# Kernel optimization log

Measured on AMD Instinct MI355X. Metric: run time of the kernel, lower is better.

## Reference

```python
import jax, jax.numpy as jnp
import numpy as np

SLOPE = 25.0   # fast_sigmoid surrogate slope
BETA = 0.9     # LIF decay
THR = 1.0      # snntorch default threshold
STEPS = 10


@jax.custom_vjp
def spike(x):
    # Heaviside forward, fast-sigmoid surrogate backward
    return (x > 0).astype(x.dtype)

def _spike_fwd(x):
    return spike(x), x

def _spike_bwd(x, g):
    return (g / (SLOPE * jnp.abs(x) + 1.0) ** 2,)

spike.defvjp(_spike_fwd, _spike_bwd)


def lif(inp, mem):
    # snntorch Leaky, reset_mechanism='subtract': reset based on previous mem, detached
    reset = jax.lax.stop_gradient((mem > THR).astype(mem.dtype))
    mem = BETA * mem + inp - reset * THR
    spk = spike(mem - THR)
    return spk, mem


def setup_inputs() -> dict:
    key = jax.random.key(0)
    ks = jax.random.split(key, 4)
    B, IN, H, O = 65536, 512, 1024, 1
    x = jax.random.normal(ks[0], (B, IN), dtype=jnp.float32)
    W1 = jax.random.normal(ks[1], (IN, H), dtype=jnp.float32) / np.sqrt(IN)
    b1 = jnp.zeros((H,), jnp.float32)
    W2 = jax.random.normal(ks[2], (H, H), dtype=jnp.float32) / np.sqrt(H)
    b2 = jnp.zeros((H,), jnp.float32)
    Wo = jax.random.normal(ks[3], (H, O), dtype=jnp.float32) / np.sqrt(H)
    bo = jnp.zeros((O,), jnp.float32)
    return {"x": x, "W1": W1, "b1": b1, "W2": W2, "b2": b2, "Wo": Wo, "bo": bo}


def reference(x, W1, b1, W2, b2, Wo, bo):
    # fc1(x) is identical every timestep (x is static input current)
    cur1 = x @ W1 + b1                      # [B, H]
    B = x.shape[0]
    H = W1.shape[1]
    O = Wo.shape[1]
    m1 = jnp.zeros((B, H), x.dtype)
    m2 = jnp.zeros((B, H), x.dtype)
    mo = jnp.zeros((B, O), x.dtype)

    def step(carry, _):
        m1, m2, mo = carry
        s1, m1 = lif(cur1, m1)
        s2, m2 = lif(s1 @ W2 + b2, m2)
        _, mo = lif(s2 @ Wo + bo, mo)
        return (m1, m2, mo), mo

    _, recs = jax.lax.scan(step, (m1, m2, mo), None, length=STEPS)  # [STEPS, B, O]
    return recs.mean(0)
```

## Files before the change

kernel.cpp:

```cpp
#include <hip/hip_runtime.h>
#include <cstdint>
#include <cstddef>


typedef _Float16 f16;
typedef _Float16 f16x8 __attribute__((ext_vector_type(8)));
typedef float f32x4 __attribute__((ext_vector_type(4)));
typedef int i32x4 __attribute__((ext_vector_type(4)));

#define MFMA16(A, B, C) __builtin_amdgcn_mfma_f32_16x16x32_f16(A, B, C, 0, 0, 0)

static constexpr int BSZ = 65536;
static constexpr int IN = 512;
static constexpr int H = 1024;

__global__ void prep_dekker(const float* __restrict__ src, f16* __restrict__ dst) {
    int idx = blockIdx.x * 256 + threadIdx.x;
    int k = idx >> 10;
    int j = idx & 1023;
    float w = src[(size_t)k * 1024 + j];
    f16 hi = (f16)w;
    float lo = (w - (float)hi) * 2048.0f;
    size_t o = (size_t)j * 1024 + k;
    dst[o] = hi;
    dst[o + (size_t)H * H] = (f16)lo;
}

__global__ __launch_bounds__(256, 2) void k1_chain(
    const float* __restrict__ x, const float* __restrict__ w1,
    const float* __restrict__ b1, unsigned short* __restrict__ s1b) {
    __shared__ float xs[32][132];
    __shared__ float ws[32][256];
    const int hblk = blockIdx.x;
    const int bblk = blockIdx.y;
    const int tid = threadIdx.x;
    const int ht = tid & 15, bt = tid >> 4;
    const int h0 = hblk * 256, b0 = bblk * 128;

    float acc[8][16] = {};

    float4 xv[4], wv[8];
#pragma unroll
    for (int i = 0; i < 4; ++i) {
        int idx = tid + 256 * i;
        int br = idx >> 3, ks = idx & 7;
        xv[i] = *(const float4*)&x[(size_t)(b0 + br) * IN + ks * 4];
    }
#pragma unroll
    for (int i = 0; i < 8; ++i) {
        int idx = tid + 256 * i;
        int kr = idx >> 6, c4 = idx & 63;
        wv[i] = *(const float4*)&w1[(size_t)kr * H + h0 + c4 * 4];
    }

    for (int kc = 0; kc < 512; kc += 32) {
        __syncthreads();
#pragma unroll
        for (int i = 0; i < 4; ++i) {
            int idx = tid + 256 * i;
            int br = idx >> 3, ks = idx & 7;
            xs[ks * 4 + 0][br] = xv[i].x;
            xs[ks * 4 + 1][br] = xv[i].y;
            xs[ks * 4 + 2][br] = xv[i].z;
            xs[ks * 4 + 3][br] = xv[i].w;
        }
#pragma unroll
        for (int i = 0; i < 8; ++i) {
            int idx = tid + 256 * i;
            int kr = idx >> 6, c4 = idx & 63;
            *(float4*)&ws[kr][c4 * 4] = wv[i];
        }
        __syncthreads();
        int kn = (kc + 32) & 511;
#pragma unroll
        for (int i = 0; i < 4; ++i) {
            int idx = tid + 256 * i;
            int br = idx >> 3, ks = idx & 7;
            xv[i] = *(const float4*)&x[(size_t)(b0 + br) * IN + kn + ks * 4];
        }
#pragma unroll
        for (int i = 0; i < 8; ++i) {
            int idx = tid + 256 * i;
            int kr = idx >> 6, c4 = idx & 63;
            wv[i] = *(const float4*)&w1[(size_t)(kn + kr) * H + h0 + c4 * 4];
        }
#pragma unroll 2
        for (int k = 0; k < 32; ++k) {
            float xr[8];
            *(float4*)&xr[0] = *(const float4*)&xs[k][bt * 8];
            *(float4*)&xr[4] = *(const float4*)&xs[k][bt * 8 + 4];
            float wr[16];
#pragma unroll
            for (int g = 0; g < 4; ++g)
                *(float4*)&wr[g * 4] = *(const float4*)&ws[k][ht * 4 + 64 * g];
#pragma unroll
            for (int i = 0; i < 8; ++i)
#pragma unroll
                for (int j = 0; j < 16; ++j)
                    acc[i][j] = fmaf(xr[i], wr[j], acc[i][j]);
        }
    }

    float b1v[16];
#pragma unroll
    for (int g = 0; g < 4; ++g)
#pragma unroll
        for (int m = 0; m < 4; ++m)
            b1v[g * 4 + m] = b1[h0 + g * 64 + ht * 4 + m];
#pragma unroll
    for (int i = 0; i < 8; ++i) {
        unsigned short outb[16];
#pragma unroll
        for (int j = 0; j < 16; ++j) {
            float c = __fadd_rn(acc[i][j], b1v[j]);
            float m = 0.0f;
            unsigned bits = 0u;
#pragma unroll
            for (int t = 0; t < 10; ++t) {
                float rst = (m > 1.0f) ? 1.0f : 0.0f;
                m = __fmul_rn(0.9f, m);
                m = __fadd_rn(m, c);
                m = __fsub_rn(m, rst);
                if (m > 1.0f) bits |= (1u << t);
            }
            outb[j] = (unsigned short)bits;
        }
        size_t row = (size_t)(b0 + bt * 8 + i);
#pragma unroll
        for (int g = 0; g < 4; ++g)
            *(int2*)&s1b[row * H + h0 + g * 64 + ht * 4] = ((const int2*)outb)[g];
    }
}

__global__ __launch_bounds__(512, 4) void k2_spikes_gemm(
    const unsigned short* __restrict__ s1bits, const f16* __restrict__ w2d,
    const float* __restrict__ b2, const float* __restrict__ wo,
    float* __restrict__ po) {
    __shared__ i32x4 AL[2][2][4][64];
    __shared__ i32x4 BL[2][2][2][2][64];
    __shared__ float m2x[4][64][8];
    const int jblk = blockIdx.x, bblk = blockIdx.y;
    const int tid = threadIdx.x;
    const int lane = tid & 63, wave = tid >> 6;
    const int strip = wave & 3, thalf = wave >> 2;
    const int l15 = lane & 15, loct = lane >> 4;
    const int t0 = thalf * 5;

    const bool stageB = (tid >= 256);
    const int s = tid & 255;
    const int sl15 = s & 15, sseg = (s >> 4) & 3;
    const int slot = (sseg << 4) | sl15;
    const int astrip = s >> 6;
    const int bp = (s >> 7) & 1, bcf = (s >> 6) & 1;

    const char* gsrc;
    if (stageB)
        gsrc = (const char*)(w2d + (size_t)bp * H * H
                             + (size_t)(jblk * 32 + bcf * 16 + sl15) * 1024 + sseg * 8);
    else
        gsrc = (const char*)(s1bits + (size_t)(bblk * 64 + astrip * 16 + sl15) * 1024 + sseg * 8);

    f32x4 acc[5][2][2] = {};

    i32x4 gv0 = *(const i32x4*)(gsrc);
    i32x4 gv1 = *(const i32x4*)(gsrc + 64);

    typedef union { i32x4 i; unsigned long long u[2]; f16x8 h; } U;

    int buf = 0;
    for (int kc = 0; kc < 1024; kc += 64) {
        if (stageB) {
            BL[buf][0][bp][bcf][slot] = gv0;
            BL[buf][1][bp][bcf][slot] = gv1;
        } else {
            AL[buf][0][astrip][slot] = gv0;
            AL[buf][1][astrip][slot] = gv1;
        }
        int kn = (kc + 64) & 1023;
        i32x4 gn0 = *(const i32x4*)(gsrc + kn * 2);
        i32x4 gn1 = *(const i32x4*)(gsrc + kn * 2 + 64);
        asm volatile("s_waitcnt lgkmcnt(0)" ::: "memory");
        __builtin_amdgcn_s_barrier();
#pragma unroll
        for (int kch = 0; kch < 2; ++kch) {
            U m;
            m.i = AL[buf][kch][strip][lane];
            f16x8 bf[2][2];
#pragma unroll
            for (int p = 0; p < 2; ++p)
#pragma unroll
                for (int cf = 0; cf < 2; ++cf) {
                    U b; b.i = BL[buf][kch][p][cf][lane];
                    bf[p][cf] = b.h;
                }
#pragma unroll
            for (int tt = 0; tt < 5; ++tt) {
                const int sh = 10 - (t0 + tt);
                U r;
                r.u[0] = (m.u[0] << sh) & 0x0400040004000400ULL;
                r.u[1] = (m.u[1] << sh) & 0x0400040004000400ULL;
                acc[tt][0][0] = MFMA16(r.h, bf[0][0], acc[tt][0][0]);
                acc[tt][0][1] = MFMA16(r.h, bf[0][1], acc[tt][0][1]);
                acc[tt][1][0] = MFMA16(r.h, bf[1][0], acc[tt][1][0]);
                acc[tt][1][1] = MFMA16(r.h, bf[1][1], acc[tt][1][1]);
            }
        }
        gv0 = gn0; gv1 = gn1;
        buf ^= 1;
    }

    int col0 = jblk * 32 + l15;
    float b2v0 = b2[col0], b2v1 = b2[col0 + 16];
    double wov0 = (double)wo[col0], wov1 = (double)wo[col0 + 16];
    int rowb = bblk * 64 + strip * 16 + loct * 4;
    float m2a[4] = {0.0f, 0.0f, 0.0f, 0.0f};
    float m2b[4] = {0.0f, 0.0f, 0.0f, 0.0f};

    if (thalf == 0) {
#pragma unroll
        for (int tt = 0; tt < 5; ++tt) {
#pragma unroll
            for (int r = 0; r < 4; ++r) {
                float i0 = (float)((double)acc[tt][0][0][r] * 16384.0 + (double)acc[tt][1][0][r] * 8.0);
                i0 = __fadd_rn(i0, b2v0);
                float rst0 = (m2a[r] > 1.0f) ? 1.0f : 0.0f;
                m2a[r] = __fmul_rn(0.9f, m2a[r]);
                m2a[r] = __fadd_rn(m2a[r], i0);
                m2a[r] = __fsub_rn(m2a[r], rst0);
                float i1 = (float)((double)acc[tt][0][1][r] * 16384.0 + (double)acc[tt][1][1][r] * 8.0);
                i1 = __fadd_rn(i1, b2v1);
                float rst1 = (m2b[r] > 1.0f) ? 1.0f : 0.0f;
                m2b[r] = __fmul_rn(0.9f, m2b[r]);
                m2b[r] = __fadd_rn(m2b[r], i1);
                m2b[r] = __fsub_rn(m2b[r], rst1);
                double pv = ((m2a[r] > 1.0f) ? wov0 : 0.0) + ((m2b[r] > 1.0f) ? wov1 : 0.0);
                pv += __shfl_xor(pv, 1);
                pv += __shfl_xor(pv, 2);
                pv += __shfl_xor(pv, 4);
                pv += __shfl_xor(pv, 8);
                if (l15 == r)
                    po[(size_t)(tt * 32 + jblk) * BSZ + rowb + r] = (float)pv;
            }
        }
#pragma unroll
        for (int r = 0; r < 4; ++r) {
            m2x[strip][lane][r] = m2a[r];
            m2x[strip][lane][4 + r] = m2b[r];
        }
    }
    __syncthreads();
    if (thalf == 1) {
#pragma unroll
        for (int r = 0; r < 4; ++r) {
            m2a[r] = m2x[strip][lane][r];
            m2b[r] = m2x[strip][lane][4 + r];
        }
#pragma unroll
        for (int tt = 0; tt < 5; ++tt) {
#pragma unroll
            for (int r = 0; r < 4; ++r) {
                float i0 = (float)((double)acc[tt][0][0][r] * 16384.0 + (double)acc[tt][1][0][r] * 8.0);
                i0 = __fadd_rn(i0, b2v0);
                float rst0 = (m2a[r] > 1.0f) ? 1.0f : 0.0f;
                m2a[r] = __fmul_rn(0.9f, m2a[r]);
                m2a[r] = __fadd_rn(m2a[r], i0);
                m2a[r] = __fsub_rn(m2a[r], rst0);
                float i1 = (float)((double)acc[tt][0][1][r] * 16384.0 + (double)acc[tt][1][1][r] * 8.0);
                i1 = __fadd_rn(i1, b2v1);
                float rst1 = (m2b[r] > 1.0f) ? 1.0f : 0.0f;
                m2b[r] = __fmul_rn(0.9f, m2b[r]);
                m2b[r] = __fadd_rn(m2b[r], i1);
                m2b[r] = __fsub_rn(m2b[r], rst1);
                double pv = ((m2a[r] > 1.0f) ? wov0 : 0.0) + ((m2b[r] > 1.0f) ? wov1 : 0.0);
                pv += __shfl_xor(pv, 1);
                pv += __shfl_xor(pv, 2);
                pv += __shfl_xor(pv, 4);
                pv += __shfl_xor(pv, 8);
                if (l15 == r)
                    po[(size_t)((5 + tt) * 32 + jblk) * BSZ + rowb + r] = (float)pv;
            }
        }
    }
}

__global__ void k3_out(const float* __restrict__ po, const float* __restrict__ bo,
                       float* __restrict__ out) {
    int b = blockIdx.x * 256 + threadIdx.x;
    float mo = 0.0f, s = 0.0f;
    float bov = bo[0];
    for (int t = 0; t < 10; ++t) {
        float inp = 0.0f;
#pragma unroll
        for (int jb = 0; jb < 32; ++jb) inp += po[(size_t)(t * 32 + jb) * BSZ + b];
        inp = __fadd_rn(inp, bov);
        float rst = (mo > 1.0f) ? 1.0f : 0.0f;
        mo = __fmul_rn(0.9f, mo);
        mo = __fadd_rn(mo, inp);
        mo = __fsub_rn(mo, rst);
        s += mo;
    }
    out[b] = s / 10.0f;
}

extern "C" void kernel_launch(void* const* d_in, const int* in_sizes, int n_in,
                              void* d_out, int out_size, void* d_ws, size_t ws_size,
                              hipStream_t stream) {
    (void)in_sizes; (void)n_in; (void)out_size; (void)ws_size;
    const float* x  = (const float*)d_in[0];
    const float* W1 = (const float*)d_in[1];
    const float* b1 = (const float*)d_in[2];
    const float* W2 = (const float*)d_in[3];
    const float* b2 = (const float*)d_in[4];
    const float* Wo = (const float*)d_in[5];
    const float* bo = (const float*)d_in[6];
    float* out = (float*)d_out;

    char* ws = (char*)d_ws;
    f16* w2d = (f16*)ws;
    unsigned short* s1bits = (unsigned short*)(ws + ((size_t)16 << 20));
    float* po = (float*)(ws + ((size_t)160 << 20));

    prep_dekker<<<dim3((H * H) / 256), 256, 0, stream>>>(W2, w2d);
    k1_chain<<<dim3(4, BSZ / 128), 256, 0, stream>>>(x, W1, b1, s1bits);
    k2_spikes_gemm<<<dim3(H / 32, BSZ / 64), 512, 0, stream>>>(s1bits, w2d, b2, Wo, po);
    k3_out<<<dim3(BSZ / 256), 256, 0, stream>>>(po, bo, out);
}
```

Before: 3.108 ms.

## Use direct global-to-LDS loads and give each wave all ten timesteps in spike GEMM

The spike GEMM kernel now stages A and B tiles with global_load_lds instead of register round-trips through dedicated staging threads. Each of four waves computes all ten timesteps, doubling the accumulators per wave and halving the block to 256 threads. This removes the LDS handoff of membrane state between the two timestep halves and the __syncthreads that went with it. The cost is heavy register pressure (160 accumulator VGPRs), which lowers occupancy, and each wave now processes the timesteps serially.

```diff
diff --git a/kernel.cpp b/kernel.cpp
--- a/kernel.cpp
+++ b/kernel.cpp
@@ -7,12 +7,19 @@
 typedef _Float16 f16x8 __attribute__((ext_vector_type(8)));
 typedef float f32x4 __attribute__((ext_vector_type(4)));
 typedef int i32x4 __attribute__((ext_vector_type(4)));
+typedef unsigned int u32;
 
 #define MFMA16(A, B, C) __builtin_amdgcn_mfma_f32_16x16x32_f16(A, B, C, 0, 0, 0)
 
 static constexpr int BSZ = 65536;
 static constexpr int IN = 512;
 static constexpr int H = 1024;
+
+__device__ __forceinline__ void gl_lds16(const void* g, void* l) {
+    __builtin_amdgcn_global_load_lds(
+        (const __attribute__((address_space(1))) u32*)g,
+        (__attribute__((address_space(3))) u32*)l, 16, 0, 0);
+}
 
 __global__ void prep_dekker(const float* __restrict__ src, f16* __restrict__ dst) {
     int idx = blockIdx.x * 256 + threadIdx.x;
@@ -132,59 +139,45 @@
     }
 }
 
-__global__ __launch_bounds__(512, 4) void k2_spikes_gemm(
+__global__ __launch_bounds__(256, 2) void k2_spikes_gemm(
     const unsigned short* __restrict__ s1bits, const f16* __restrict__ w2d,
     const float* __restrict__ b2, const float* __restrict__ wo,
     float* __restrict__ po) {
     __shared__ i32x4 AL[2][2][4][64];
     __shared__ i32x4 BL[2][2][2][2][64];
-    __shared__ float m2x[4][64][8];
     const int jblk = blockIdx.x, bblk = blockIdx.y;
     const int tid = threadIdx.x;
     const int lane = tid & 63, wave = tid >> 6;
-    const int strip = wave & 3, thalf = wave >> 2;
     const int l15 = lane & 15, loct = lane >> 4;
-    const int t0 = thalf * 5;
-
-    const bool stageB = (tid >= 256);
-    const int s = tid & 255;
-    const int sl15 = s & 15, sseg = (s >> 4) & 3;
-    const int slot = (sseg << 4) | sl15;
-    const int astrip = s >> 6;
-    const int bp = (s >> 7) & 1, bcf = (s >> 6) & 1;
-
-    const char* gsrc;
-    if (stageB)
-        gsrc = (const char*)(w2d + (size_t)bp * H * H
-                             + (size_t)(jblk * 32 + bcf * 16 + sl15) * 1024 + sseg * 8);
-    else
-        gsrc = (const char*)(s1bits + (size_t)(bblk * 64 + astrip * 16 + sl15) * 1024 + sseg * 8);
-
-    f32x4 acc[5][2][2] = {};
-
-    i32x4 gv0 = *(const i32x4*)(gsrc);
-    i32x4 gv1 = *(const i32x4*)(gsrc + 64);
+    const int bpW = wave >> 1, bcfW = wave & 1;
+
+    const unsigned short* gA =
+        s1bits + (size_t)(bblk * 64 + wave * 16 + l15) * 1024 + loct * 8;
+    const f16* gB = w2d + (size_t)bpW * H * H
+                  + (size_t)(jblk * 32 + bcfW * 16 + l15) * 1024 + loct * 8;
+
+    f32x4 acc[10][2][2] = {};
+
+    gl_lds16(gA,      &AL[0][0][wave][0]);
+    gl_lds16(gA + 32, &AL[0][1][wave][0]);
+    gl_lds16(gB,      &BL[0][0][bpW][bcfW][0]);
+    gl_lds16(gB + 32, &BL[0][1][bpW][bcfW][0]);
+    asm volatile("s_waitcnt vmcnt(0)" ::: "memory");
+    __builtin_amdgcn_s_barrier();
 
     typedef union { i32x4 i; unsigned long long u[2]; f16x8 h; } U;
 
     int buf = 0;
     for (int kc = 0; kc < 1024; kc += 64) {
-        if (stageB) {
-            BL[buf][0][bp][bcf][slot] = gv0;
-            BL[buf][1][bp][bcf][slot] = gv1;
-        } else {
-            AL[buf][0][astrip][slot] = gv0;
-            AL[buf][1][astrip][slot] = gv1;
-        }
-        int kn = (kc + 64) & 1023;
-        i32x4 gn0 = *(const i32x4*)(gsrc + kn * 2);
-        i32x4 gn1 = *(const i32x4*)(gsrc + kn * 2 + 64);
-        asm volatile("s_waitcnt lgkmcnt(0)" ::: "memory");
-        __builtin_amdgcn_s_barrier();
+        const int kn = (kc + 64) & 1023;
+        gl_lds16(gA + kn,      &AL[buf ^ 1][0][wave][0]);
+        gl_lds16(gA + kn + 32, &AL[buf ^ 1][1][wave][0]);
+        gl_lds16(gB + kn,      &BL[buf ^ 1][0][bpW][bcfW][0]);
+        gl_lds16(gB + kn + 32, &BL[buf ^ 1][1][bpW][bcfW][0]);
 #pragma unroll
         for (int kch = 0; kch < 2; ++kch) {
             U m;
-            m.i = AL[buf][kch][strip][lane];
+            m.i = AL[buf][kch][wave][lane];
             f16x8 bf[2][2];
 #pragma unroll
             for (int p = 0; p < 2; ++p)
@@ -194,8 +187,8 @@
                     bf[p][cf] = b.h;
                 }
 #pragma unroll
-            for (int tt = 0; tt < 5; ++tt) {
-                const int sh = 10 - (t0 + tt);
+            for (int tt = 0; tt < 10; ++tt) {
+                const int sh = 10 - tt;
                 U r;
                 r.u[0] = (m.u[0] << sh) & 0x0400040004000400ULL;
                 r.u[1] = (m.u[1] << sh) & 0x0400040004000400ULL;
@@ -205,80 +198,41 @@
                 acc[tt][1][1] = MFMA16(r.h, bf[1][1], acc[tt][1][1]);
             }
         }
-        gv0 = gn0; gv1 = gn1;
+        asm volatile("s_waitcnt vmcnt(0)" ::: "memory");
+        __builtin_amdgcn_s_barrier();
         buf ^= 1;
     }
 
     int col0 = jblk * 32 + l15;
     float b2v0 = b2[col0], b2v1 = b2[col0 + 16];
     double wov0 = (double)wo[col0], wov1 = (double)wo[col0 + 16];
-    int rowb = bblk * 64 + strip * 16 + loct * 4;
+    int rowb = bblk * 64 + wave * 16 + loct * 4;
     float m2a[4] = {0.0f, 0.0f, 0.0f, 0.0f};
     float m2b[4] = {0.0f, 0.0f, 0.0f, 0.0f};
 
-    if (thalf == 0) {
-#pragma unroll
-        for (int tt = 0; tt < 5; ++tt) {
-#pragma unroll
-            for (int r = 0; r < 4; ++r) {
-                float i0 = (float)((double)acc[tt][0][0][r] * 16384.0 + (double)acc[tt][1][0][r] * 8.0);
-                i0 = __fadd_rn(i0, b2v0);
-                float rst0 = (m2a[r] > 1.0f) ? 1.0f : 0.0f;
-                m2a[r] = __fmul_rn(0.9f, m2a[r]);
-                m2a[r] = __fadd_rn(m2a[r], i0);
-                m2a[r] = __fsub_rn(m2a[r], rst0);
-                float i1 = (float)((double)acc[tt][0][1][r] * 16384.0 + (double)acc[tt][1][1][r] * 8.0);
-                i1 = __fadd_rn(i1, b2v1);
-                float rst1 = (m2b[r] > 1.0f) ? 1.0f : 0.0f;
-                m2b[r] = __fmul_rn(0.9f, m2b[r]);
-                m2b[r] = __fadd_rn(m2b[r], i1);
-                m2b[r] = __fsub_rn(m2b[r], rst1);
-                double pv = ((m2a[r] > 1.0f) ? wov0 : 0.0) + ((m2b[r] > 1.0f) ? wov1 : 0.0);
-                pv += __shfl_xor(pv, 1);
-                pv += __shfl_xor(pv, 2);
-                pv += __shfl_xor(pv, 4);
-                pv += __shfl_xor(pv, 8);
-                if (l15 == r)
-                    po[(size_t)(tt * 32 + jblk) * BSZ + rowb + r] = (float)pv;
-            }
-        }
+#pragma unroll
+    for (int tt = 0; tt < 10; ++tt) {
 #pragma unroll
         for (int r = 0; r < 4; ++r) {
-            m2x[strip][lane][r] = m2a[r];
-            m2x[strip][lane][4 + r] = m2b[r];
-        }
-    }
-    __syncthreads();
-    if (thalf == 1) {
-#pragma unroll
-        for (int r = 0; r < 4; ++r) {
-            m2a[r] = m2x[strip][lane][r];
-            m2b[r] = m2x[strip][lane][4 + r];
-        }
-#pragma unroll
-        for (int tt = 0; tt < 5; ++tt) {
-#pragma unroll
-            for (int r = 0; r < 4; ++r) {
-                float i0 = (float)((double)acc[tt][0][0][r] * 16384.0 + (double)acc[tt][1][0][r] * 8.0);
-                i0 = __fadd_rn(i0, b2v0);
-                float rst0 = (m2a[r] > 1.0f) ? 1.0f : 0.0f;
-                m2a[r] = __fmul_rn(0.9f, m2a[r]);
-                m2a[r] = __fadd_rn(m2a[r], i0);
-                m2a[r] = __fsub_rn(m2a[r], rst0);
-                float i1 = (float)((double)acc[tt][0][1][r] * 16384.0 + (double)acc[tt][1][1][r] * 8.0);
-                i1 = __fadd_rn(i1, b2v1);
-                float rst1 = (m2b[r] > 1.0f) ? 1.0f : 0.0f;
-                m2b[r] = __fmul_rn(0.9f, m2b[r]);
-                m2b[r] = __fadd_rn(m2b[r], i1);
-                m2b[r] = __fsub_rn(m2b[r], rst1);
-                double pv = ((m2a[r] > 1.0f) ? wov0 : 0.0) + ((m2b[r] > 1.0f) ? wov1 : 0.0);
-                pv += __shfl_xor(pv, 1);
-                pv += __shfl_xor(pv, 2);
-                pv += __shfl_xor(pv, 4);
-                pv += __shfl_xor(pv, 8);
-                if (l15 == r)
-                    po[(size_t)((5 + tt) * 32 + jblk) * BSZ + rowb + r] = (float)pv;
-            }
+            float i0 = (float)((double)acc[tt][0][0][r] * 16384.0 + (double)acc[tt][1][0][r] * 8.0);
+            i0 = __fadd_rn(i0, b2v0);
+            float rst0 = (m2a[r] > 1.0f) ? 1.0f : 0.0f;
+            m2a[r] = __fmul_rn(0.9f, m2a[r]);
+            m2a[r] = __fadd_rn(m2a[r], i0);
+            m2a[r] = __fsub_rn(m2a[r], rst0);
+            float i1 = (float)((double)acc[tt][0][1][r] * 16384.0 + (double)acc[tt][1][1][r] * 8.0);
+            i1 = __fadd_rn(i1, b2v1);
+            float rst1 = (m2b[r] > 1.0f) ? 1.0f : 0.0f;
+            m2b[r] = __fmul_rn(0.9f, m2b[r]);
+            m2b[r] = __fadd_rn(m2b[r], i1);
+            m2b[r] = __fsub_rn(m2b[r], rst1);
+            double pv = ((m2a[r] > 1.0f) ? wov0 : 0.0) + ((m2b[r] > 1.0f) ? wov1 : 0.0);
+            pv += __shfl_xor(pv, 1);
+            pv += __shfl_xor(pv, 2);
+            pv += __shfl_xor(pv, 4);
+            pv += __shfl_xor(pv, 8);
+            if (l15 == r)
+                po[(size_t)(tt * 32 + jblk) * BSZ + rowb + r] = (float)pv;
         }
     }
 }
@@ -322,6 +276,6 @@
 
     prep_dekker<<<dim3((H * H) / 256), 256, 0, stream>>>(W2, w2d);
     k1_chain<<<dim3(4, BSZ / 128), 256, 0, stream>>>(x, W1, b1, s1bits);
-    k2_spikes_gemm<<<dim3(H / 32, BSZ / 64), 512, 0, stream>>>(s1bits, w2d, b2, Wo, po);
+    k2_spikes_gemm<<<dim3(H / 32, BSZ / 64), 256, 0, stream>>>(s1bits, w2d, b2, Wo, po);
     k3_out<<<dim3(BSZ / 256), 256, 0, stream>>>(po, bo, out);
 }
```

Result: slower. 3.578 ms (+15.1%).

## Stage k2 operands via direct global-to-LDS loads with triple buffering

Applied to the files above, without the earlier changes.

Replaces the register-staged double-buffered LDS fill in the spike GEMM with direct global_load_lds transfers into a three-deep ring of LDS buffers, issued two stages ahead and gated by vmcnt waits. This removes the register round trip and the separate LDS writes, and lets more global loads overlap the MFMA work. It also raises wave priority around the MFMA burst and aliases the epilogue scratch onto the same LDS allocation. LDS per block grows, which may lower occupancy, and correctness depends on the vmcnt counts and barriers ordering the ring buffer reuse properly.

```diff
diff --git a/kernel.cpp b/kernel.cpp
--- a/kernel.cpp
+++ b/kernel.cpp
@@ -7,12 +7,19 @@
 typedef _Float16 f16x8 __attribute__((ext_vector_type(8)));
 typedef float f32x4 __attribute__((ext_vector_type(4)));
 typedef int i32x4 __attribute__((ext_vector_type(4)));
+typedef unsigned int u32;
 
 #define MFMA16(A, B, C) __builtin_amdgcn_mfma_f32_16x16x32_f16(A, B, C, 0, 0, 0)
 
 static constexpr int BSZ = 65536;
 static constexpr int IN = 512;
 static constexpr int H = 1024;
+
+__device__ __forceinline__ void gl_lds16(const void* g, void* l) {
+    __builtin_amdgcn_global_load_lds(
+        (const __attribute__((address_space(1))) u32*)g,
+        (__attribute__((address_space(3))) u32*)l, 16, 0, 0);
+}
 
 __global__ void prep_dekker(const float* __restrict__ src, f16* __restrict__ dst) {
     int idx = blockIdx.x * 256 + threadIdx.x;
@@ -136,9 +143,11 @@
     const unsigned short* __restrict__ s1bits, const f16* __restrict__ w2d,
     const float* __restrict__ b2, const float* __restrict__ wo,
     float* __restrict__ po) {
-    __shared__ i32x4 AL[2][2][4][64];
-    __shared__ i32x4 BL[2][2][2][2][64];
-    __shared__ float m2x[4][64][8];
+    __shared__ __align__(16) char ldsraw[49152];
+    i32x4 (*AL)[2][4][64]    = (i32x4 (*)[2][4][64])ldsraw;
+    i32x4 (*BL)[2][2][2][64] = (i32x4 (*)[2][2][2][64])(ldsraw + 24576);
+    float (*m2x)[64][8]      = (float (*)[64][8])ldsraw;
+
     const int jblk = blockIdx.x, bblk = blockIdx.y;
     const int tid = threadIdx.x;
     const int lane = tid & 63, wave = tid >> 6;
@@ -146,53 +155,51 @@
     const int l15 = lane & 15, loct = lane >> 4;
     const int t0 = thalf * 5;
 
-    const bool stageB = (tid >= 256);
-    const int s = tid & 255;
-    const int sl15 = s & 15, sseg = (s >> 4) & 3;
-    const int slot = (sseg << 4) | sl15;
-    const int astrip = s >> 6;
-    const int bp = (s >> 7) & 1, bcf = (s >> 6) & 1;
-
-    const char* gsrc;
-    if (stageB)
-        gsrc = (const char*)(w2d + (size_t)bp * H * H
-                             + (size_t)(jblk * 32 + bcf * 16 + sl15) * 1024 + sseg * 8);
-    else
-        gsrc = (const char*)(s1bits + (size_t)(bblk * 64 + astrip * 16 + sl15) * 1024 + sseg * 8);
+    const bool stB = (wave >= 4);
+    const int bp = (wave >> 1) & 1, bcf = wave & 1;
+    const unsigned short* gA =
+        s1bits + (size_t)(bblk * 64 + strip * 16 + l15) * 1024 + loct * 8;
+    const f16* gB = w2d + (size_t)bp * H * H
+                  + (size_t)(jblk * 32 + bcf * 16 + l15) * 1024 + loct * 8;
 
     f32x4 acc[5][2][2] = {};
 
-    i32x4 gv0 = *(const i32x4*)(gsrc);
-    i32x4 gv1 = *(const i32x4*)(gsrc + 64);
-
     typedef union { i32x4 i; unsigned long long u[2]; f16x8 h; } U;
 
-    int buf = 0;
-    for (int kc = 0; kc < 1024; kc += 64) {
-        if (stageB) {
-            BL[buf][0][bp][bcf][slot] = gv0;
-            BL[buf][1][bp][bcf][slot] = gv1;
-        } else {
-            AL[buf][0][astrip][slot] = gv0;
-            AL[buf][1][astrip][slot] = gv1;
-        }
-        int kn = (kc + 64) & 1023;
-        i32x4 gn0 = *(const i32x4*)(gsrc + kn * 2);
-        i32x4 gn1 = *(const i32x4*)(gsrc + kn * 2 + 64);
-        asm volatile("s_waitcnt lgkmcnt(0)" ::: "memory");
-        __builtin_amdgcn_s_barrier();
+#define STAGE(t_)                                                        \
+    do {                                                                 \
+        int bi_ = (t_) % 3;                                              \
+        int kk_ = ((t_) * 64) & 1023;                                    \
+        if (stB) {                                                       \
+            gl_lds16(gB + kk_,      &BL[bi_][0][bp][bcf][0]);            \
+            gl_lds16(gB + kk_ + 32, &BL[bi_][1][bp][bcf][0]);            \
+        } else {                                                         \
+            gl_lds16(gA + kk_,      &AL[bi_][0][strip][0]);              \
+            gl_lds16(gA + kk_ + 32, &AL[bi_][1][strip][0]);              \
+        }                                                                \
+    } while (0)
+
+    STAGE(0);
+    STAGE(1);
+    asm volatile("s_waitcnt vmcnt(2)" ::: "memory");
+    __builtin_amdgcn_s_barrier();
+
+    for (int t = 0; t < 16; ++t) {
+        const int bi = t % 3;
+        STAGE(t + 2);
 #pragma unroll
         for (int kch = 0; kch < 2; ++kch) {
             U m;
-            m.i = AL[buf][kch][strip][lane];
+            m.i = AL[bi][kch][strip][lane];
             f16x8 bf[2][2];
 #pragma unroll
             for (int p = 0; p < 2; ++p)
 #pragma unroll
                 for (int cf = 0; cf < 2; ++cf) {
-                    U b; b.i = BL[buf][kch][p][cf][lane];
+                    U b; b.i = BL[bi][kch][p][cf][lane];
                     bf[p][cf] = b.h;
                 }
+            __builtin_amdgcn_s_setprio(1);
 #pragma unroll
             for (int tt = 0; tt < 5; ++tt) {
                 const int sh = 10 - (t0 + tt);
@@ -204,10 +211,12 @@
                 acc[tt][1][0] = MFMA16(r.h, bf[1][0], acc[tt][1][0]);
                 acc[tt][1][1] = MFMA16(r.h, bf[1][1], acc[tt][1][1]);
             }
-        }
-        gv0 = gn0; gv1 = gn1;
-        buf ^= 1;
-    }
+            __builtin_amdgcn_s_setprio(0);
+        }
+        asm volatile("s_waitcnt vmcnt(2)" ::: "memory");
+        __builtin_amdgcn_s_barrier();
+    }
+#undef STAGE
 
     int col0 = jblk * 32 + l15;
     float b2v0 = b2[col0], b2v1 = b2[col0 + 16];
```

Result: no change. 3.168 ms (+1.9%).
